# Optimization experiments

Hardware: AMD Instinct MI355X
Metric: run time of the kernel (lower is better)

Reference implementation:

```python
import jax, jax.numpy as jnp
import numpy as np

TOP_K = 2  # config.num_experts_per_tok


def setup_inputs() -> dict:
    key = jax.random.key(0)
    ks = jax.random.split(key, 5)
    B, S, H, F, E = 1, 2048, 2048, 1408, 8
    sc_h = 1.0 / np.sqrt(H)
    sc_f = 1.0 / np.sqrt(F)
    return {
        "hidden_states": jax.random.normal(ks[0], (B, S, H), jnp.float32),
        "gate_w": jax.random.normal(ks[1], (E, H), jnp.float32) * sc_h,
        "w1": jax.random.normal(ks[2], (E, F, H), jnp.float32) * sc_h,
        "w3": jax.random.normal(ks[3], (E, F, H), jnp.float32) * sc_h,
        "w2": jax.random.normal(ks[4], (E, H, F), jnp.float32) * sc_f,
    }


def reference(hidden_states, gate_w, w1, w3, w2):
    B, S, H = hidden_states.shape
    x = hidden_states.reshape(-1, H)            # [T, H]
    T = x.shape[0]
    E = gate_w.shape[0]

    # Router: logits -> fp32 softmax -> top-k -> renormalize
    router_logits = x @ gate_w.T                # [T, E]
    probs = jax.nn.softmax(router_logits.astype(jnp.float32), axis=-1)
    topk_w, topk_idx = jax.lax.top_k(probs, TOP_K)          # [T, K]
    topk_w = topk_w / topk_w.sum(axis=-1, keepdims=True)
    topk_w = topk_w.astype(x.dtype)

    # Scatter top-k weights into a dense [T, E] combine matrix (zero elsewhere)
    w_full = jnp.zeros((T, E), x.dtype).at[jnp.arange(T)[:, None], topk_idx].add(topk_w)

    # Per-expert SwiGLU MLP applied to all tokens; masked combine honors routing.
    g = jnp.einsum('th,efh->etf', x, w1)        # [E, T, F]
    u = jnp.einsum('th,efh->etf', x, w3)        # [E, T, F]
    h = jax.nn.silu(g) * u                      # [E, T, F]
    y = jnp.einsum('etf,ehf->eth', h, w2)       # [E, T, H]
    out = jnp.einsum('eth,te->th', y, w_full)   # [T, H]

    final_hidden_states = out.reshape(B, S, H)
    return final_hidden_states, router_logits
```

## Files before the change

kernel.cpp:

```cpp
#include <hip/hip_runtime.h>
#include <hip/hip_bf16.h>

#define T_TOK 2048
#define H_DIM 2048
#define F_DIM 1408
#define N_EXP 8
#define BM 128
#define BN 64
#define BK 64

#define NITEM 40
#define G1_NY (F_DIM / BN)
#define G2_NY (H_DIM / BN)
#define G1_CHUNK ((NITEM * G1_NY) / 8)
#define G2_CHUNK ((NITEM * G2_NY) / 8)

typedef float f32x4 __attribute__((ext_vector_type(4)));
typedef short s16x8 __attribute__((ext_vector_type(8)));
typedef unsigned int u32;

#define LOFF(row, kbyte) (((row) << 7) + ((kbyte) ^ (((row) & 7) << 4)))

__device__ __forceinline__ int bf2i(__hip_bfloat162 h) {
  int r; __builtin_memcpy(&r, &h, 4); return r;
}

__device__ __forceinline__ int4 pack8(float4 a, float4 b) {
  int4 r;
  r.x = bf2i(__float22bfloat162_rn(float2{a.x, a.y}));
  r.y = bf2i(__float22bfloat162_rn(float2{a.z, a.w}));
  r.z = bf2i(__float22bfloat162_rn(float2{b.x, b.y}));
  r.w = bf2i(__float22bfloat162_rn(float2{b.z, b.w}));
  return r;
}

__device__ __forceinline__ unsigned short f2bf(float f) {
  __hip_bfloat16 h = __float2bfloat16(f);
  unsigned short r; __builtin_memcpy(&r, &h, 2); return r;
}

__device__ __forceinline__ f32x4 mfma16(s16x8 a, s16x8 b, f32x4 c) {
  return __builtin_amdgcn_mfma_f32_16x16x32_bf16(a, b, c, 0, 0, 0);
}

__device__ __forceinline__ void dma16(const unsigned short* g, unsigned short* l) {
  __builtin_amdgcn_global_load_lds((const __attribute__((address_space(1))) u32*)g,
                                   (__attribute__((address_space(3))) u32*)l, 16, 0, 0);
}

__global__ void router_kernel(const float* __restrict__ x, const float* __restrict__ gw,
                              float* __restrict__ logits, int* __restrict__ tk_idx,
                              float* __restrict__ tk_w, unsigned short* __restrict__ xb) {
  __shared__ float xs[H_DIM];
  __shared__ float lg[N_EXP];
  const int t = blockIdx.x;
  const int tid = threadIdx.x;
  const float4 xv = ((const float4*)(x + (size_t)t * H_DIM))[tid];
  ((float4*)xs)[tid] = xv;
  int2 cw;
  cw.x = bf2i(__float22bfloat162_rn(float2{xv.x, xv.y}));
  cw.y = bf2i(__float22bfloat162_rn(float2{xv.z, xv.w}));
  ((int2*)(xb + (size_t)t * H_DIM))[tid] = cw;
  __syncthreads();
  const int w = tid >> 6, l = tid & 63;
  const float* g = gw + w * H_DIM;
  float s = 0.f;
  for (int j = l; j < H_DIM; j += 64) s += xs[j] * g[j];
#pragma unroll
  for (int o = 32; o; o >>= 1) s += __shfl_down(s, o);
  if (l == 0) lg[w] = s;
  __syncthreads();
  if (tid == 0) {
    float mx = lg[0];
#pragma unroll
    for (int i = 1; i < N_EXP; i++) mx = fmaxf(mx, lg[i]);
    float p[N_EXP];
#pragma unroll
    for (int i = 0; i < N_EXP; i++) p[i] = __expf(lg[i] - mx);
    int i0 = 0;
#pragma unroll
    for (int i = 1; i < N_EXP; i++) if (p[i] > p[i0]) i0 = i;
    int i1 = (i0 == 0) ? 1 : 0;
#pragma unroll
    for (int i = 0; i < N_EXP; i++) if (i != i0 && p[i] > p[i1]) i1 = i;
    const float ww = p[i0] + p[i1];
    tk_idx[t * 2] = i0; tk_idx[t * 2 + 1] = i1;
    tk_w[t * 2] = p[i0] / ww; tk_w[t * 2 + 1] = p[i1] / ww;
#pragma unroll
    for (int i = 0; i < N_EXP; i++) logits[t * N_EXP + i] = lg[i];
  }
}

__global__ void build_lists(const int* __restrict__ tk_idx, const float* __restrict__ tk_w,
                            int* __restrict__ counts, int* __restrict__ entries,
                            float* __restrict__ wlist) {
  const int e = blockIdx.x;
  const int l = threadIdx.x;
  int base = 0;
  for (int t0 = 0; t0 < T_TOK; t0 += 64) {
    const int t = t0 + l;
    int sel = -1; float w = 0.f;
    const int i0 = tk_idx[t * 2], i1 = tk_idx[t * 2 + 1];
    if (i0 == e) { sel = t * 2; w = tk_w[t * 2]; }
    else if (i1 == e) { sel = t * 2 + 1; w = tk_w[t * 2 + 1]; }
    const unsigned long long mask = __ballot(sel >= 0);
    const int pos = base + __popcll(mask & ((1ull << l) - 1ull));
    if (sel >= 0) { entries[e * T_TOK + pos] = sel; wlist[e * T_TOK + pos] = w; }
    base += __popcll(mask);
  }
  if (l == 0) counts[e] = base;
}

__global__ void build_items(const int* __restrict__ counts, int* __restrict__ items) {
  if (threadIdx.x == 0) {
    int n = 0;
#pragma unroll
    for (int e = 0; e < N_EXP; e++) {
      const int c = counts[e];
      for (int m0 = 0; m0 < c; m0 += BM) items[1 + n++] = (e << 16) | (m0 / BM);
    }
    items[0] = n;
  }
}

#define G1_STEP(ARD, AWR, BLR1, BLW1, BLR3, BLW3, RS1, RS3, KA1_, KB3_)       \
  {                                                                           \
    asm volatile("s_waitcnt vmcnt(4) lgkmcnt(0)" ::: "memory");               \
    __builtin_amdgcn_s_barrier();                                             \
    *(int4*)((BLW1) + offB) = pack8(RS1[0], RS1[1]);                          \
    *(int4*)((BLW3) + offB) = pack8(RS3[0], RS3[1]);                          \
    {                                                                         \
      const int ka = (KA1_);                                                  \
      dma16(ga0 + ka, (AWR) + aw);                                            \
      dma16(ga1 + ka, (AWR) + aw + 512);                                      \
      const int kbl = (KB3_);                                                 \
      RS1[0] = *(const float4*)(pb1 + kbl);                                   \
      RS1[1] = *(const float4*)(pb1 + kbl + 4);                               \
      RS3[0] = *(const float4*)(pb3 + kbl);                                   \
      RS3[1] = *(const float4*)(pb3 + kbl + 4);                               \
    }                                                                         \
    __builtin_amdgcn_sched_barrier(0);                                        \
    __builtin_amdgcn_s_setprio(1);                                            \
    _Pragma("unroll")                                                         \
    for (int kk = 0; kk < 2; kk++) {                                          \
      const int kbyte = kk * 64 + kb;                                         \
      const s16x8 a0 = *(const s16x8*)((const char*)(ARD) + LOFF(rowA0, kbyte)); \
      const s16x8 a1 = *(const s16x8*)((const char*)(ARD) + LOFF(rowA1, kbyte)); \
      const s16x8 p0 = *(const s16x8*)((BLR1) + LOFF(rowB0, kbyte));          \
      const s16x8 p1 = *(const s16x8*)((BLR1) + LOFF(rowB1, kbyte));          \
      const s16x8 q0 = *(const s16x8*)((BLR3) + LOFF(rowB0, kbyte));          \
      const s16x8 q1 = *(const s16x8*)((BLR3) + LOFF(rowB1, kbyte));          \
      aG[0][0] = mfma16(a0, p0, aG[0][0]); aG[0][1] = mfma16(a0, p1, aG[0][1]); \
      aG[1][0] = mfma16(a1, p0, aG[1][0]); aG[1][1] = mfma16(a1, p1, aG[1][1]); \
      aU[0][0] = mfma16(a0, q0, aU[0][0]); aU[0][1] = mfma16(a0, q1, aU[0][1]); \
      aU[1][0] = mfma16(a1, q0, aU[1][0]); aU[1][1] = mfma16(a1, q1, aU[1][1]); \
    }                                                                         \
    __builtin_amdgcn_s_setprio(0);                                            \
  }

__global__ __launch_bounds__(512)
void moe_gemm1(const float* __restrict__ w1, const float* __restrict__ w3,
               const unsigned short* __restrict__ xb,
               const int* __restrict__ counts, const int* __restrict__ entries,
               const int* __restrict__ items,
               unsigned short* __restrict__ hb) {
  const int lin = blockIdx.x;
  const int virt = (lin & 7) * G1_CHUNK + (lin >> 3);
  const int ix = virt % NITEM;
  const int iy = virt / NITEM;
  if (ix >= items[0]) return;
  const int it = items[1 + ix];
  const int e = it >> 16;
  const int m0 = (it & 0xffff) * BM;
  const int rem = counts[e] - m0;
  const int n0 = iy * BN;

  __shared__ unsigned short sA[2][BM * BK];
  __shared__ unsigned short sB1[2][BN * BK];
  __shared__ unsigned short sB3[2][BN * BK];
  char* sb10 = (char*)sB1[0]; char* sb11 = (char*)sB1[1];
  char* sb30 = (char*)sB3[0]; char* sb31 = (char*)sB3[1];

  const int tid = threadIdx.x;
  const int lane = tid & 63;
  const int wave = tid >> 6;
  const int wm = wave >> 1, wn = wave & 1;

  const int* elist = entries + e * T_TOK + m0;

  const int r0 = tid >> 3;
  const int gc = tid & 7;
  const float* pb1 = w1 + ((size_t)e * F_DIM + n0 + r0) * H_DIM + gc * 8;
  const float* pb3 = w3 + ((size_t)e * F_DIM + n0 + r0) * H_DIM + gc * 8;
  const int offB = LOFF(r0, gc * 16);

  const int arow0 = wave * 16 + (lane >> 3);
  const int arow1 = arow0 + 8;
  const int gcolb = (((lane & 7) << 4) ^ (((lane >> 3) & 7) << 4));
  const int tokA0 = elist[arow0 < rem ? arow0 : 0] >> 1;
  const int tokA1 = elist[arow1 < rem ? arow1 : 0] >> 1;
  const unsigned short* ga0 = xb + (size_t)tokA0 * H_DIM + (gcolb >> 1);
  const unsigned short* ga1 = xb + (size_t)tokA1 * H_DIM + (gcolb >> 1);
  const int aw = wave * 1024;

  const int rowA0 = wm * 32 + (lane & 15);
  const int rowA1 = rowA0 + 16;
  const int rowB0 = wn * 32 + (lane & 15);
  const int rowB1 = rowB0 + 16;
  const int kb = (lane >> 4) * 16;

  const f32x4 zero = {0.f, 0.f, 0.f, 0.f};
  f32x4 aG[2][2], aU[2][2];
#pragma unroll
  for (int i = 0; i < 2; i++)
#pragma unroll
    for (int j = 0; j < 2; j++) { aG[i][j] = zero; aU[i][j] = zero; }

  float4 s1_1[2], s1_3[2], s0_1[2], s0_3[2];
  s1_1[0] = *(const float4*)(pb1);      s1_1[1] = *(const float4*)(pb1 + 4);
  s1_3[0] = *(const float4*)(pb3);      s1_3[1] = *(const float4*)(pb3 + 4);
  s0_1[0] = *(const float4*)(pb1 + BK); s0_1[1] = *(const float4*)(pb1 + BK + 4);
  s0_3[0] = *(const float4*)(pb3 + BK); s0_3[1] = *(const float4*)(pb3 + BK + 4);
  dma16(ga0, sA[0] + aw);
  dma16(ga1, sA[0] + aw + 512);
  asm volatile("s_waitcnt vmcnt(6)" ::: "memory");
  *(int4*)(sb10 + offB) = pack8(s1_1[0], s1_1[1]);
  *(int4*)(sb30 + offB) = pack8(s1_3[0], s1_3[1]);
  s1_1[0] = *(const float4*)(pb1 + 2 * BK); s1_1[1] = *(const float4*)(pb1 + 2 * BK + 4);
  s1_3[0] = *(const float4*)(pb3 + 2 * BK); s1_3[1] = *(const float4*)(pb3 + 2 * BK + 4);

  const int NT = H_DIM / BK;
  for (int t = 0; t < NT; t += 2) {
    const int ka1 = (t + 1 < NT) ? (t + 1) * BK : 0;
    const int ka2 = (t + 2 < NT) ? (t + 2) * BK : 0;
    const int kb3 = (t + 3 < NT) ? (t + 3) * BK : 0;
    const int kb4 = (t + 4 < NT) ? (t + 4) * BK : 0;
    G1_STEP(sA[0], sA[1], sb10, sb11, sb30, sb31, s0_1, s0_3, ka1, kb3);
    G1_STEP(sA[1], sA[0], sb11, sb10, sb31, sb30, s1_1, s1_3, ka2, kb4);
  }

#pragma unroll
  for (int i = 0; i < 2; i++) {
#pragma unroll
    for (int r = 0; r < 4; r++) {
      const int m = wm * 32 + i * 16 + ((lane >> 4) << 2) + r;
      if (m < rem) {
        const int entry = elist[m];
        unsigned short* hp = hb + (size_t)entry * F_DIM + n0 + wn * 32 + (lane & 15);
#pragma unroll
        for (int j = 0; j < 2; j++) {
          const float g = aG[i][j][r];
          const float u = aU[i][j][r];
          hp[j * 16] = f2bf(g / (1.f + __expf(-g)) * u);
        }
      }
    }
  }
}

#define G2_STEP(ARD, AWR, BLR, BLW, RS, KA1_, KB3_)                           \
  {                                                                           \
    asm volatile("s_waitcnt vmcnt(2) lgkmcnt(0)" ::: "memory");               \
    __builtin_amdgcn_s_barrier();                                             \
    *(int4*)((BLW) + offB) = pack8(RS[0], RS[1]);                             \
    {                                                                         \
      const int ka = (KA1_);                                                  \
      dma16(ga0 + ka, (AWR) + aw);                                            \
      dma16(ga1 + ka, (AWR) + aw + 512);                                      \
      const int kbl = (KB3_);                                                 \
      RS[0] = *(const float4*)(pb + kbl);                                     \
      RS[1] = *(const float4*)(pb + kbl + 4);                                 \
    }                                                                         \
    __builtin_amdgcn_sched_barrier(0);                                        \
    __builtin_amdgcn_s_setprio(1);                                            \
    _Pragma("unroll")                                                         \
    for (int kk = 0; kk < 2; kk++) {                                          \
      const int kbyte = kk * 64 + kb;                                         \
      const s16x8 a0 = *(const s16x8*)((const char*)(ARD) + LOFF(rowA0, kbyte)); \
      const s16x8 a1 = *(const s16x8*)((const char*)(ARD) + LOFF(rowA1, kbyte)); \
      const s16x8 f0 = *(const s16x8*)((BLR) + LOFF(rowB0, kbyte));           \
      const s16x8 f1 = *(const s16x8*)((BLR) + LOFF(rowB1, kbyte));           \
      ac[0][0] = mfma16(a0, f0, ac[0][0]); ac[0][1] = mfma16(a0, f1, ac[0][1]); \
      ac[1][0] = mfma16(a1, f0, ac[1][0]); ac[1][1] = mfma16(a1, f1, ac[1][1]); \
    }                                                                         \
    __builtin_amdgcn_s_setprio(0);                                            \
  }

__global__ __launch_bounds__(512)
void moe_gemm2(const float* __restrict__ w2,
               const unsigned short* __restrict__ hb,
               const int* __restrict__ counts, const int* __restrict__ entries,
               const float* __restrict__ wlist, const int* __restrict__ items,
               float* __restrict__ out) {
  const int lin = blockIdx.x;
  const int virt = (lin & 7) * G2_CHUNK + (lin >> 3);
  const int ix = virt % NITEM;
  const int iy = virt / NITEM;
  if (ix >= items[0]) return;
  const int it = items[1 + ix];
  const int e = it >> 16;
  const int m0 = (it & 0xffff) * BM;
  const int rem = counts[e] - m0;
  const int n0 = iy * BN;

  __shared__ unsigned short sA[2][BM * BK];
  __shared__ unsigned short sB[2][BN * BK];
  char* sb0 = (char*)sB[0]; char* sb1 = (char*)sB[1];

  const int tid = threadIdx.x;
  const int lane = tid & 63;
  const int wave = tid >> 6;
  const int wm = wave >> 1, wn = wave & 1;

  const int* elist = entries + e * T_TOK + m0;
  const float* wl = wlist + e * T_TOK + m0;

  const int r0 = tid >> 3;
  const int gc = tid & 7;
  const float* pb = w2 + ((size_t)e * H_DIM + n0 + r0) * F_DIM + gc * 8;
  const int offB = LOFF(r0, gc * 16);

  const int arow0 = wave * 16 + (lane >> 3);
  const int arow1 = arow0 + 8;
  const int gcolb = (((lane & 7) << 4) ^ (((lane >> 3) & 7) << 4));
  const int enA0 = elist[arow0 < rem ? arow0 : 0];
  const int enA1 = elist[arow1 < rem ? arow1 : 0];
  const unsigned short* ga0 = hb + (size_t)enA0 * F_DIM + (gcolb >> 1);
  const unsigned short* ga1 = hb + (size_t)enA1 * F_DIM + (gcolb >> 1);
  const int aw = wave * 1024;

  const int rowA0 = wm * 32 + (lane & 15);
  const int rowA1 = rowA0 + 16;
  const int rowB0 = wn * 32 + (lane & 15);
  const int rowB1 = rowB0 + 16;
  const int kb = (lane >> 4) * 16;

  const f32x4 zero = {0.f, 0.f, 0.f, 0.f};
  f32x4 ac[2][2];
#pragma unroll
  for (int i = 0; i < 2; i++)
#pragma unroll
    for (int j = 0; j < 2; j++) ac[i][j] = zero;

  float4 s1r[2], s0r[2];
  s1r[0] = *(const float4*)(pb);      s1r[1] = *(const float4*)(pb + 4);
  s0r[0] = *(const float4*)(pb + BK); s0r[1] = *(const float4*)(pb + BK + 4);
  dma16(ga0, sA[0] + aw);
  dma16(ga1, sA[0] + aw + 512);
  asm volatile("s_waitcnt vmcnt(4)" ::: "memory");
  *(int4*)(sb0 + offB) = pack8(s1r[0], s1r[1]);
  s1r[0] = *(const float4*)(pb + 2 * BK); s1r[1] = *(const float4*)(pb + 2 * BK + 4);

  const int NT = F_DIM / BK;
  for (int t = 0; t < NT; t += 2) {
    const int ka1 = (t + 1 < NT) ? (t + 1) * BK : 0;
    const int ka2 = (t + 2 < NT) ? (t + 2) * BK : 0;
    const int kb3 = (t + 3 < NT) ? (t + 3) * BK : 0;
    const int kb4 = (t + 4 < NT) ? (t + 4) * BK : 0;
    G2_STEP(sA[0], sA[1], sb0, sb1, s0r, ka1, kb3);
    G2_STEP(sA[1], sA[0], sb1, sb0, s1r, ka2, kb4);
  }

#pragma unroll
  for (int i = 0; i < 2; i++) {
#pragma unroll
    for (int r = 0; r < 4; r++) {
      const int m = wm * 32 + i * 16 + ((lane >> 4) << 2) + r;
      if (m < rem) {
        const int entry = elist[m];
        const int tok = entry >> 1;
        const float wgt = wl[m];
        float* op = out + (size_t)tok * H_DIM + n0 + wn * 32 + (lane & 15);
#pragma unroll
        for (int j = 0; j < 2; j++) atomicAdd(op + j * 16, wgt * ac[i][j][r]);
      }
    }
  }
}

extern "C" void kernel_launch(void* const* d_in, const int* in_sizes, int n_in,
                              void* d_out, int out_size, void* d_ws, size_t ws_size,
                              hipStream_t stream) {
  const float* x  = (const float*)d_in[0];
  const float* gw = (const float*)d_in[1];
  const float* w1 = (const float*)d_in[2];
  const float* w3 = (const float*)d_in[3];
  const float* w2 = (const float*)d_in[4];
  float* out = (float*)d_out;
  float* logits = out + (size_t)T_TOK * H_DIM;

  char* ws = (char*)d_ws;
  size_t off = 0;
  unsigned short* xb = (unsigned short*)(ws + off); off += (size_t)T_TOK * H_DIM * 2;
  unsigned short* hb = (unsigned short*)(ws + off); off += (size_t)T_TOK * 2 * F_DIM * 2;
  int*   tk_idx = (int*)(ws + off);   off += (size_t)T_TOK * 2 * 4;
  float* tk_w   = (float*)(ws + off); off += (size_t)T_TOK * 2 * 4;
  int*   counts = (int*)(ws + off);   off += 256;
  int*   entries = (int*)(ws + off);  off += (size_t)N_EXP * T_TOK * 4;
  float* wlist  = (float*)(ws + off); off += (size_t)N_EXP * T_TOK * 4;
  int*   items  = (int*)(ws + off);   off += 256;

  (void)hipMemsetAsync(d_out, 0, (size_t)out_size * sizeof(float), stream);
  router_kernel<<<dim3(T_TOK), 512, 0, stream>>>(x, gw, logits, tk_idx, tk_w, xb);
  build_lists<<<dim3(N_EXP), 64, 0, stream>>>(tk_idx, tk_w, counts, entries, wlist);
  build_items<<<dim3(1), 64, 0, stream>>>(counts, items);
  moe_gemm1<<<dim3(NITEM * G1_NY), 512, 0, stream>>>(w1, w3, xb, counts, entries, items, hb);
  moe_gemm2<<<dim3(NITEM * G2_NY), 512, 0, stream>>>(w2, hb, counts, entries, wlist, items, out);
}
```

Baseline: 234.2 us.

## Replace A-tile LDS DMA with register-staged prefetch in both MoE GEMMs

Result: slower. 454.7 us (+94.1%).

```diff
diff --git a/kernel.cpp b/kernel.cpp
--- a/kernel.cpp
+++ b/kernel.cpp
@@ -41,11 +41,6 @@
 
 __device__ __forceinline__ f32x4 mfma16(s16x8 a, s16x8 b, f32x4 c) {
   return __builtin_amdgcn_mfma_f32_16x16x32_bf16(a, b, c, 0, 0, 0);
-}
-
-__device__ __forceinline__ void dma16(const unsigned short* g, unsigned short* l) {
-  __builtin_amdgcn_global_load_lds((const __attribute__((address_space(1))) u32*)g,
-                                   (__attribute__((address_space(3))) u32*)l, 16, 0, 0);
 }
 
 __global__ void router_kernel(const float* __restrict__ x, const float* __restrict__ gw,
@@ -123,33 +118,34 @@
   }
 }
 
-#define G1_STEP(ARD, AWR, BLR1, BLW1, BLR3, BLW3, RS1, RS3, KA1_, KB3_)       \
+#define G1_STEP(ARD, AWR, BR1, BW1, BR3, BW3, AS, BS1, BS3, KN_)              \
   {                                                                           \
-    asm volatile("s_waitcnt vmcnt(4) lgkmcnt(0)" ::: "memory");               \
+    asm volatile("s_waitcnt vmcnt(6) lgkmcnt(0)" ::: "memory");               \
     __builtin_amdgcn_s_barrier();                                             \
-    *(int4*)((BLW1) + offB) = pack8(RS1[0], RS1[1]);                          \
-    *(int4*)((BLW3) + offB) = pack8(RS3[0], RS3[1]);                          \
+    *(int4*)((AWR) + offA0) = AS[0];                                          \
+    *(int4*)((AWR) + offA1) = AS[1];                                          \
+    *(int4*)((BW1) + offB) = pack8(BS1[0], BS1[1]);                           \
+    *(int4*)((BW3) + offB) = pack8(BS3[0], BS3[1]);                           \
     {                                                                         \
-      const int ka = (KA1_);                                                  \
-      dma16(ga0 + ka, (AWR) + aw);                                            \
-      dma16(ga1 + ka, (AWR) + aw + 512);                                      \
-      const int kbl = (KB3_);                                                 \
-      RS1[0] = *(const float4*)(pb1 + kbl);                                   \
-      RS1[1] = *(const float4*)(pb1 + kbl + 4);                               \
-      RS3[0] = *(const float4*)(pb3 + kbl);                                   \
-      RS3[1] = *(const float4*)(pb3 + kbl + 4);                               \
+      const int kn = (KN_);                                                   \
+      AS[0] = *(const int4*)(gaA + kn);                                       \
+      AS[1] = *(const int4*)(gaA + kn + 8);                                   \
+      BS1[0] = *(const float4*)(pb1 + kn);                                    \
+      BS1[1] = *(const float4*)(pb1 + kn + 4);                                \
+      BS3[0] = *(const float4*)(pb3 + kn);                                    \
+      BS3[1] = *(const float4*)(pb3 + kn + 4);                                \
     }                                                                         \
     __builtin_amdgcn_sched_barrier(0);                                        \
     __builtin_amdgcn_s_setprio(1);                                            \
     _Pragma("unroll")                                                         \
     for (int kk = 0; kk < 2; kk++) {                                          \
       const int kbyte = kk * 64 + kb;                                         \
-      const s16x8 a0 = *(const s16x8*)((const char*)(ARD) + LOFF(rowA0, kbyte)); \
-      const s16x8 a1 = *(const s16x8*)((const char*)(ARD) + LOFF(rowA1, kbyte)); \
-      const s16x8 p0 = *(const s16x8*)((BLR1) + LOFF(rowB0, kbyte));          \
-      const s16x8 p1 = *(const s16x8*)((BLR1) + LOFF(rowB1, kbyte));          \
-      const s16x8 q0 = *(const s16x8*)((BLR3) + LOFF(rowB0, kbyte));          \
-      const s16x8 q1 = *(const s16x8*)((BLR3) + LOFF(rowB1, kbyte));          \
+      const s16x8 a0 = *(const s16x8*)((ARD) + LOFF(rowA0, kbyte));           \
+      const s16x8 a1 = *(const s16x8*)((ARD) + LOFF(rowA1, kbyte));           \
+      const s16x8 p0 = *(const s16x8*)((BR1) + LOFF(rowB0, kbyte));           \
+      const s16x8 p1 = *(const s16x8*)((BR1) + LOFF(rowB1, kbyte));           \
+      const s16x8 q0 = *(const s16x8*)((BR3) + LOFF(rowB0, kbyte));           \
+      const s16x8 q1 = *(const s16x8*)((BR3) + LOFF(rowB1, kbyte));           \
       aG[0][0] = mfma16(a0, p0, aG[0][0]); aG[0][1] = mfma16(a0, p1, aG[0][1]); \
       aG[1][0] = mfma16(a1, p0, aG[1][0]); aG[1][1] = mfma16(a1, p1, aG[1][1]); \
       aU[0][0] = mfma16(a0, q0, aU[0][0]); aU[0][1] = mfma16(a0, q1, aU[0][1]); \
@@ -178,6 +174,7 @@
   __shared__ unsigned short sA[2][BM * BK];
   __shared__ unsigned short sB1[2][BN * BK];
   __shared__ unsigned short sB3[2][BN * BK];
+  char* sa0 = (char*)sA[0]; char* sa1 = (char*)sA[1];
   char* sb10 = (char*)sB1[0]; char* sb11 = (char*)sB1[1];
   char* sb30 = (char*)sB3[0]; char* sb31 = (char*)sB3[1];
 
@@ -194,14 +191,12 @@
   const float* pb3 = w3 + ((size_t)e * F_DIM + n0 + r0) * H_DIM + gc * 8;
   const int offB = LOFF(r0, gc * 16);
 
-  const int arow0 = wave * 16 + (lane >> 3);
-  const int arow1 = arow0 + 8;
-  const int gcolb = (((lane & 7) << 4) ^ (((lane >> 3) & 7) << 4));
-  const int tokA0 = elist[arow0 < rem ? arow0 : 0] >> 1;
-  const int tokA1 = elist[arow1 < rem ? arow1 : 0] >> 1;
-  const unsigned short* ga0 = xb + (size_t)tokA0 * H_DIM + (gcolb >> 1);
-  const unsigned short* ga1 = xb + (size_t)tokA1 * H_DIM + (gcolb >> 1);
-  const int aw = wave * 1024;
+  const int r0a = tid >> 2;
+  const int gc4 = tid & 3;
+  const int tokA = elist[r0a < rem ? r0a : 0] >> 1;
+  const unsigned short* gaA = xb + (size_t)tokA * H_DIM + gc4 * 16;
+  const int offA0 = LOFF(r0a, gc4 * 32);
+  const int offA1 = LOFF(r0a, gc4 * 32 + 16);
 
   const int rowA0 = wm * 32 + (lane & 15);
   const int rowA1 = rowA0 + 16;
@@ -216,27 +211,29 @@
 #pragma unroll
     for (int j = 0; j < 2; j++) { aG[i][j] = zero; aU[i][j] = zero; }
 
-  float4 s1_1[2], s1_3[2], s0_1[2], s0_3[2];
-  s1_1[0] = *(const float4*)(pb1);      s1_1[1] = *(const float4*)(pb1 + 4);
-  s1_3[0] = *(const float4*)(pb3);      s1_3[1] = *(const float4*)(pb3 + 4);
-  s0_1[0] = *(const float4*)(pb1 + BK); s0_1[1] = *(const float4*)(pb1 + BK + 4);
-  s0_3[0] = *(const float4*)(pb3 + BK); s0_3[1] = *(const float4*)(pb3 + BK + 4);
-  dma16(ga0, sA[0] + aw);
-  dma16(ga1, sA[0] + aw + 512);
-  asm volatile("s_waitcnt vmcnt(6)" ::: "memory");
-  *(int4*)(sb10 + offB) = pack8(s1_1[0], s1_1[1]);
-  *(int4*)(sb30 + offB) = pack8(s1_3[0], s1_3[1]);
-  s1_1[0] = *(const float4*)(pb1 + 2 * BK); s1_1[1] = *(const float4*)(pb1 + 2 * BK + 4);
-  s1_3[0] = *(const float4*)(pb3 + 2 * BK); s1_3[1] = *(const float4*)(pb3 + 2 * BK + 4);
+  int4 A0[2], A1r[2];
+  float4 B0_1[2], B0_3[2], B1_1[2], B1_3[2];
+  A0[0] = *(const int4*)(gaA);      A0[1] = *(const int4*)(gaA + 8);
+  B0_1[0] = *(const float4*)(pb1);  B0_1[1] = *(const float4*)(pb1 + 4);
+  B0_3[0] = *(const float4*)(pb3);  B0_3[1] = *(const float4*)(pb3 + 4);
+  asm volatile("s_waitcnt vmcnt(0)" ::: "memory");
+  *(int4*)(sa0 + offA0) = A0[0];
+  *(int4*)(sa0 + offA1) = A0[1];
+  *(int4*)(sb10 + offB) = pack8(B0_1[0], B0_1[1]);
+  *(int4*)(sb30 + offB) = pack8(B0_3[0], B0_3[1]);
+  A0[0] = *(const int4*)(gaA + BK);      A0[1] = *(const int4*)(gaA + BK + 8);
+  B0_1[0] = *(const float4*)(pb1 + BK);  B0_1[1] = *(const float4*)(pb1 + BK + 4);
+  B0_3[0] = *(const float4*)(pb3 + BK);  B0_3[1] = *(const float4*)(pb3 + BK + 4);
+  A1r[0] = *(const int4*)(gaA + 2 * BK);      A1r[1] = *(const int4*)(gaA + 2 * BK + 8);
+  B1_1[0] = *(const float4*)(pb1 + 2 * BK);   B1_1[1] = *(const float4*)(pb1 + 2 * BK + 4);
+  B1_3[0] = *(const float4*)(pb3 + 2 * BK);   B1_3[1] = *(const float4*)(pb3 + 2 * BK + 4);
 
   const int NT = H_DIM / BK;
   for (int t = 0; t < NT; t += 2) {
-    const int ka1 = (t + 1 < NT) ? (t + 1) * BK : 0;
-    const int ka2 = (t + 2 < NT) ? (t + 2) * BK : 0;
-    const int kb3 = (t + 3 < NT) ? (t + 3) * BK : 0;
-    const int kb4 = (t + 4 < NT) ? (t + 4) * BK : 0;
-    G1_STEP(sA[0], sA[1], sb10, sb11, sb30, sb31, s0_1, s0_3, ka1, kb3);
-    G1_STEP(sA[1], sA[0], sb11, sb10, sb31, sb30, s1_1, s1_3, ka2, kb4);
+    const int kn0 = (t + 3 < NT) ? (t + 3) * BK : 0;
+    const int kn1 = (t + 4 < NT) ? (t + 4) * BK : 0;
+    G1_STEP(sa0, sa1, sb10, sb11, sb30, sb31, A0, B0_1, B0_3, kn0);
+    G1_STEP(sa1, sa0, sb11, sb10, sb31, sb30, A1r, B1_1, B1_3, kn1);
   }
 
 #pragma unroll
@@ -258,28 +255,29 @@
   }
 }
 
-#define G2_STEP(ARD, AWR, BLR, BLW, RS, KA1_, KB3_)                           \
+#define G2_STEP(ARD, AWR, BR, BW, AS, BS, KN_)                                \
   {                                                                           \
-    asm volatile("s_waitcnt vmcnt(2) lgkmcnt(0)" ::: "memory");               \
+    asm volatile("s_waitcnt vmcnt(4) lgkmcnt(0)" ::: "memory");               \
     __builtin_amdgcn_s_barrier();                                             \
-    *(int4*)((BLW) + offB) = pack8(RS[0], RS[1]);                             \
+    *(int4*)((AWR) + offA0) = AS[0];                                          \
+    *(int4*)((AWR) + offA1) = AS[1];                                          \
+    *(int4*)((BW) + offB) = pack8(BS[0], BS[1]);                              \
     {                                                                         \
-      const int ka = (KA1_);                                                  \
-      dma16(ga0 + ka, (AWR) + aw);                                            \
-      dma16(ga1 + ka, (AWR) + aw + 512);                                      \
-      const int kbl = (KB3_);                                                 \
-      RS[0] = *(const float4*)(pb + kbl);                                     \
-      RS[1] = *(const float4*)(pb + kbl + 4);                                 \
+      const int kn = (KN_);                                                   \
+      AS[0] = *(const int4*)(gaA + kn);                                       \
+      AS[1] = *(const int4*)(gaA + kn + 8);                                   \
+      BS[0] = *(const float4*)(pb + kn);                                      \
+      BS[1] = *(const float4*)(pb + kn + 4);                                  \
     }                                                                         \
     __builtin_amdgcn_sched_barrier(0);                                        \
     __builtin_amdgcn_s_setprio(1);                                            \
     _Pragma("unroll")                                                         \
     for (int kk = 0; kk < 2; kk++) {                                          \
       const int kbyte = kk * 64 + kb;                                         \
-      const s16x8 a0 = *(const s16x8*)((const char*)(ARD) + LOFF(rowA0, kbyte)); \
-      const s16x8 a1 = *(const s16x8*)((const char*)(ARD) + LOFF(rowA1, kbyte)); \
-      const s16x8 f0 = *(const s16x8*)((BLR) + LOFF(rowB0, kbyte));           \
-      const s16x8 f1 = *(const s16x8*)((BLR) + LOFF(rowB1, kbyte));           \
+      const s16x8 a0 = *(const s16x8*)((ARD) + LOFF(rowA0, kbyte));           \
+      const s16x8 a1 = *(const s16x8*)((ARD) + LOFF(rowA1, kbyte));           \
+      const s16x8 f0 = *(const s16x8*)((BR) + LOFF(rowB0, kbyte));            \
+      const s16x8 f1 = *(const s16x8*)((BR) + LOFF(rowB1, kbyte));            \
       ac[0][0] = mfma16(a0, f0, ac[0][0]); ac[0][1] = mfma16(a0, f1, ac[0][1]); \
       ac[1][0] = mfma16(a1, f0, ac[1][0]); ac[1][1] = mfma16(a1, f1, ac[1][1]); \
     }                                                                         \
@@ -305,6 +303,7 @@
 
   __shared__ unsigned short sA[2][BM * BK];
   __shared__ unsigned short sB[2][BN * BK];
+  char* sa0 = (char*)sA[0]; char* sa1 = (char*)sA[1];
   char* sb0 = (char*)sB[0]; char* sb1 = (char*)sB[1];
 
   const int tid = threadIdx.x;
@@ -320,14 +319,12 @@
   const float* pb = w2 + ((size_t)e * H_DIM + n0 + r0) * F_DIM + gc * 8;
   const int offB = LOFF(r0, gc * 16);
 
-  const int arow0 = wave * 16 + (lane >> 3);
-  const int arow1 = arow0 + 8;
-  const int gcolb = (((lane & 7) << 4) ^ (((lane >> 3) & 7) << 4));
-  const int enA0 = elist[arow0 < rem ? arow0 : 0];
-  const int enA1 = elist[arow1 < rem ? arow1 : 0];
-  const unsigned short* ga0 = hb + (size_t)enA0 * F_DIM + (gcolb >> 1);
-  const unsigned short* ga1 = hb + (size_t)enA1 * F_DIM + (gcolb >> 1);
-  const int aw = wave * 1024;
+  const int r0a = tid >> 2;
+  const int gc4 = tid & 3;
+  const int enA = elist[r0a < rem ? r0a : 0];
+  const unsigned short* gaA = hb + (size_t)enA * F_DIM + gc4 * 16;
+  const int offA0 = LOFF(r0a, gc4 * 32);
+  const int offA1 = LOFF(r0a, gc4 * 32 + 16);
 
   const int rowA0 = wm * 32 + (lane & 15);
   const int rowA1 = rowA0 + 16;
@@ -342,23 +339,25 @@
 #pragma unroll
     for (int j = 0; j < 2; j++) ac[i][j] = zero;
 
-  float4 s1r[2], s0r[2];
-  s1r[0] = *(const float4*)(pb);      s1r[1] = *(const float4*)(pb + 4);
-  s0r[0] = *(const float4*)(pb + BK); s0r[1] = *(const float4*)(pb + BK + 4);
-  dma16(ga0, sA[0] + aw);
-  dma16(ga1, sA[0] + aw + 512);
-  asm volatile("s_waitcnt vmcnt(4)" ::: "memory");
-  *(int4*)(sb0 + offB) = pack8(s1r[0], s1r[1]);
-  s1r[0] = *(const float4*)(pb + 2 * BK); s1r[1] = *(const float4*)(pb + 2 * BK + 4);
+  int4 A0[2], A1r[2];
+  float4 B0r[2], B1r[2];
+  A0[0] = *(const int4*)(gaA);     A0[1] = *(const int4*)(gaA + 8);
+  B0r[0] = *(const float4*)(pb);   B0r[1] = *(const float4*)(pb + 4);
+  asm volatile("s_waitcnt vmcnt(0)" ::: "memory");
+  *(int4*)(sa0 + offA0) = A0[0];
+  *(int4*)(sa0 + offA1) = A0[1];
+  *(int4*)(sb0 + offB) = pack8(B0r[0], B0r[1]);
+  A0[0] = *(const int4*)(gaA + BK);      A0[1] = *(const int4*)(gaA + BK + 8);
+  B0r[0] = *(const float4*)(pb + BK);    B0r[1] = *(const float4*)(pb + BK + 4);
+  A1r[0] = *(const int4*)(gaA + 2 * BK); A1r[1] = *(const int4*)(gaA + 2 * BK + 8);
+  B1r[0] = *(const float4*)(pb + 2 * BK); B1r[1] = *(const float4*)(pb + 2 * BK + 4);
 
   const int NT = F_DIM / BK;
   for (int t = 0; t < NT; t += 2) {
-    const int ka1 = (t + 1 < NT) ? (t + 1) * BK : 0;
-    const int ka2 = (t + 2 < NT) ? (t + 2) * BK : 0;
-    const int kb3 = (t + 3 < NT) ? (t + 3) * BK : 0;
-    const int kb4 = (t + 4 < NT) ? (t + 4) * BK : 0;
-    G2_STEP(sA[0], sA[1], sb0, sb1, s0r, ka1, kb3);
-    G2_STEP(sA[1], sA[0], sb1, sb0, s1r, ka2, kb4);
+    const int kn0 = (t + 3 < NT) ? (t + 3) * BK : 0;
+    const int kn1 = (t + 4 < NT) ? (t + 4) * BK : 0;
+    G2_STEP(sa0, sa1, sb0, sb1, A0, B0r, kn0);
+    G2_STEP(sa1, sa0, sb1, sb0, A1r, B1r, kn1);
   }
 
 #pragma unroll
```

## Pre-cast expert weights to bf16 and use DMA-only grouped GEMMs

Applied to the files above, without the earlier changes.

Result: slower. 278.1 us (+18.7%).

```diff
diff --git a/kernel.cpp b/kernel.cpp
--- a/kernel.cpp
+++ b/kernel.cpp
@@ -14,6 +14,7 @@
 #define G2_NY (H_DIM / BN)
 #define G1_CHUNK ((NITEM * G1_NY) / 8)
 #define G2_CHUNK ((NITEM * G2_NY) / 8)
+#define WELEMS ((size_t)N_EXP * F_DIM * H_DIM)
 
 typedef float f32x4 __attribute__((ext_vector_type(4)));
 typedef short s16x8 __attribute__((ext_vector_type(8)));
@@ -46,6 +47,16 @@
 __device__ __forceinline__ void dma16(const unsigned short* g, unsigned short* l) {
   __builtin_amdgcn_global_load_lds((const __attribute__((address_space(1))) u32*)g,
                                    (__attribute__((address_space(3))) u32*)l, 16, 0, 0);
+}
+
+__global__ void cast_w(const float* __restrict__ in, unsigned short* __restrict__ out, int n8) {
+  int i = blockIdx.x * blockDim.x + threadIdx.x;
+  const int stride = gridDim.x * blockDim.x;
+  for (; i < n8; i += stride) {
+    const float4 a = ((const float4*)in)[2 * i];
+    const float4 b = ((const float4*)in)[2 * i + 1];
+    ((int4*)out)[i] = pack8(a, b);
+  }
 }
 
 __global__ void router_kernel(const float* __restrict__ x, const float* __restrict__ gw,
@@ -123,7 +134,225 @@
   }
 }
 
-#define G1_STEP(ARD, AWR, BLR1, BLW1, BLR3, BLW3, RS1, RS3, KA1_, KB3_)       \
+__global__ __launch_bounds__(512)
+void moe_gemm1b(const unsigned short* __restrict__ w1b, const unsigned short* __restrict__ w3b,
+                const unsigned short* __restrict__ xb,
+                const int* __restrict__ counts, const int* __restrict__ entries,
+                const int* __restrict__ items,
+                unsigned short* __restrict__ hb) {
+  const int lin = blockIdx.x;
+  const int virt = (lin & 7) * G1_CHUNK + (lin >> 3);
+  const int ix = virt % NITEM;
+  const int iy = virt / NITEM;
+  if (ix >= items[0]) return;
+  const int it = items[1 + ix];
+  const int e = it >> 16;
+  const int m0 = (it & 0xffff) * BM;
+  const int rem = counts[e] - m0;
+  const int n0 = iy * BN;
+
+  __shared__ unsigned short sA[2][BM * BK];
+  __shared__ unsigned short sB1[2][BN * BK];
+  __shared__ unsigned short sB3[2][BN * BK];
+
+  const int tid = threadIdx.x;
+  const int lane = tid & 63;
+  const int wave = tid >> 6;
+  const int wm = wave >> 1, wn = wave & 1;
+
+  const int* elist = entries + e * T_TOK + m0;
+
+  const int gcolb = (((lane & 7) << 4) ^ (((lane >> 3) & 7) << 4));
+  const int arow0 = wave * 16 + (lane >> 3);
+  const int arow1 = arow0 + 8;
+  const int tokA0 = elist[arow0 < rem ? arow0 : 0] >> 1;
+  const int tokA1 = elist[arow1 < rem ? arow1 : 0] >> 1;
+  const unsigned short* gaA0 = xb + (size_t)tokA0 * H_DIM + (gcolb >> 1);
+  const unsigned short* gaA1 = xb + (size_t)tokA1 * H_DIM + (gcolb >> 1);
+  const int awA = wave * 1024;
+
+  const int rB = tid >> 3;
+  const int gbcol = ((tid & 7) ^ (rB & 7)) * 8;
+  const unsigned short* gb1 = w1b + ((size_t)e * F_DIM + n0 + rB) * H_DIM + gbcol;
+  const unsigned short* gb3 = w3b + ((size_t)e * F_DIM + n0 + rB) * H_DIM + gbcol;
+  const int awB = wave * 512;
+
+  const int rowA0 = wm * 32 + (lane & 15);
+  const int rowA1 = rowA0 + 16;
+  const int rowB0 = wn * 32 + (lane & 15);
+  const int rowB1 = rowB0 + 16;
+  const int kb = (lane >> 4) * 16;
+
+  const f32x4 zero = {0.f, 0.f, 0.f, 0.f};
+  f32x4 aG[2][2], aU[2][2];
+#pragma unroll
+  for (int i = 0; i < 2; i++)
+#pragma unroll
+    for (int j = 0; j < 2; j++) { aG[i][j] = zero; aU[i][j] = zero; }
+
+  dma16(gaA0, sA[0] + awA);
+  dma16(gaA1, sA[0] + awA + 512);
+  dma16(gb1, sB1[0] + awB);
+  dma16(gb3, sB3[0] + awB);
+  asm volatile("s_waitcnt vmcnt(0)" ::: "memory");
+  __builtin_amdgcn_s_barrier();
+
+  const int NT = H_DIM / BK;
+  for (int t = 0; t < NT; ++t) {
+    const int cur = t & 1, nxt = cur ^ 1;
+    const int kn = (t + 1 < NT) ? (t + 1) * BK : 0;
+    dma16(gaA0 + kn, sA[nxt] + awA);
+    dma16(gaA1 + kn, sA[nxt] + awA + 512);
+    dma16(gb1 + kn, sB1[nxt] + awB);
+    dma16(gb3 + kn, sB3[nxt] + awB);
+    __builtin_amdgcn_sched_barrier(0);
+    __builtin_amdgcn_s_setprio(1);
+    const char* aC = (const char*)sA[cur];
+    const char* b1C = (const char*)sB1[cur];
+    const char* b3C = (const char*)sB3[cur];
+#pragma unroll
+    for (int kk = 0; kk < 2; kk++) {
+      const int kbyte = kk * 64 + kb;
+      const s16x8 a0 = *(const s16x8*)(aC + LOFF(rowA0, kbyte));
+      const s16x8 a1 = *(const s16x8*)(aC + LOFF(rowA1, kbyte));
+      const s16x8 p0 = *(const s16x8*)(b1C + LOFF(rowB0, kbyte));
+      const s16x8 p1 = *(const s16x8*)(b1C + LOFF(rowB1, kbyte));
+      const s16x8 q0 = *(const s16x8*)(b3C + LOFF(rowB0, kbyte));
+      const s16x8 q1 = *(const s16x8*)(b3C + LOFF(rowB1, kbyte));
+      aG[0][0] = mfma16(a0, p0, aG[0][0]); aG[0][1] = mfma16(a0, p1, aG[0][1]);
+      aG[1][0] = mfma16(a1, p0, aG[1][0]); aG[1][1] = mfma16(a1, p1, aG[1][1]);
+      aU[0][0] = mfma16(a0, q0, aU[0][0]); aU[0][1] = mfma16(a0, q1, aU[0][1]);
+      aU[1][0] = mfma16(a1, q0, aU[1][0]); aU[1][1] = mfma16(a1, q1, aU[1][1]);
+    }
+    __builtin_amdgcn_s_setprio(0);
+    asm volatile("s_waitcnt vmcnt(0) lgkmcnt(0)" ::: "memory");
+    __builtin_amdgcn_s_barrier();
+  }
+
+#pragma unroll
+  for (int i = 0; i < 2; i++) {
+#pragma unroll
+    for (int r = 0; r < 4; r++) {
+      const int m = wm * 32 + i * 16 + ((lane >> 4) << 2) + r;
+      if (m < rem) {
+        const int entry = elist[m];
+        unsigned short* hp = hb + (size_t)entry * F_DIM + n0 + wn * 32 + (lane & 15);
+#pragma unroll
+        for (int j = 0; j < 2; j++) {
+          const float g = aG[i][j][r];
+          const float u = aU[i][j][r];
+          hp[j * 16] = f2bf(g / (1.f + __expf(-g)) * u);
+        }
+      }
+    }
+  }
+}
+
+__global__ __launch_bounds__(512)
+void moe_gemm2b(const unsigned short* __restrict__ w2b,
+                const unsigned short* __restrict__ hb,
+                const int* __restrict__ counts, const int* __restrict__ entries,
+                const float* __restrict__ wlist, const int* __restrict__ items,
+                float* __restrict__ out) {
+  const int lin = blockIdx.x;
+  const int virt = (lin & 7) * G2_CHUNK + (lin >> 3);
+  const int ix = virt % NITEM;
+  const int iy = virt / NITEM;
+  if (ix >= items[0]) return;
+  const int it = items[1 + ix];
+  const int e = it >> 16;
+  const int m0 = (it & 0xffff) * BM;
+  const int rem = counts[e] - m0;
+  const int n0 = iy * BN;
+
+  __shared__ unsigned short sA[2][BM * BK];
+  __shared__ unsigned short sB[2][BN * BK];
+
+  const int tid = threadIdx.x;
+  const int lane = tid & 63;
+  const int wave = tid >> 6;
+  const int wm = wave >> 1, wn = wave & 1;
+
+  const int* elist = entries + e * T_TOK + m0;
+  const float* wl = wlist + e * T_TOK + m0;
+
+  const int gcolb = (((lane & 7) << 4) ^ (((lane >> 3) & 7) << 4));
+  const int arow0 = wave * 16 + (lane >> 3);
+  const int arow1 = arow0 + 8;
+  const int enA0 = elist[arow0 < rem ? arow0 : 0];
+  const int enA1 = elist[arow1 < rem ? arow1 : 0];
+  const unsigned short* gaA0 = hb + (size_t)enA0 * F_DIM + (gcolb >> 1);
+  const unsigned short* gaA1 = hb + (size_t)enA1 * F_DIM + (gcolb >> 1);
+  const int awA = wave * 1024;
+
+  const int rB = tid >> 3;
+  const int gbcol = ((tid & 7) ^ (rB & 7)) * 8;
+  const unsigned short* gb = w2b + ((size_t)e * H_DIM + n0 + rB) * F_DIM + gbcol;
+  const int awB = wave * 512;
+
+  const int rowA0 = wm * 32 + (lane & 15);
+  const int rowA1 = rowA0 + 16;
+  const int rowB0 = wn * 32 + (lane & 15);
+  const int rowB1 = rowB0 + 16;
+  const int kb = (lane >> 4) * 16;
+
+  const f32x4 zero = {0.f, 0.f, 0.f, 0.f};
+  f32x4 ac[2][2];
+#pragma unroll
+  for (int i = 0; i < 2; i++)
+#pragma unroll
+    for (int j = 0; j < 2; j++) ac[i][j] = zero;
+
+  dma16(gaA0, sA[0] + awA);
+  dma16(gaA1, sA[0] + awA + 512);
+  dma16(gb, sB[0] + awB);
+  asm volatile("s_waitcnt vmcnt(0)" ::: "memory");
+  __builtin_amdgcn_s_barrier();
+
+  const int NT = F_DIM / BK;
+  for (int t = 0; t < NT; ++t) {
+    const int cur = t & 1, nxt = cur ^ 1;
+    const int kn = (t + 1 < NT) ? (t + 1) * BK : 0;
+    dma16(gaA0 + kn, sA[nxt] + awA);
+    dma16(gaA1 + kn, sA[nxt] + awA + 512);
+    dma16(gb + kn, sB[nxt] + awB);
+    __builtin_amdgcn_sched_barrier(0);
+    __builtin_amdgcn_s_setprio(1);
+    const char* aC = (const char*)sA[cur];
+    const char* bC = (const char*)sB[cur];
+#pragma unroll
+    for (int kk = 0; kk < 2; kk++) {
+      const int kbyte = kk * 64 + kb;
+      const s16x8 a0 = *(const s16x8*)(aC + LOFF(rowA0, kbyte));
+      const s16x8 a1 = *(const s16x8*)(aC + LOFF(rowA1, kbyte));
+      const s16x8 f0 = *(const s16x8*)(bC + LOFF(rowB0, kbyte));
+      const s16x8 f1 = *(const s16x8*)(bC + LOFF(rowB1, kbyte));
+      ac[0][0] = mfma16(a0, f0, ac[0][0]); ac[0][1] = mfma16(a0, f1, ac[0][1]);
+      ac[1][0] = mfma16(a1, f0, ac[1][0]); ac[1][1] = mfma16(a1, f1, ac[1][1]);
+    }
+    __builtin_amdgcn_s_setprio(0);
+    asm volatile("s_waitcnt vmcnt(0) lgkmcnt(0)" ::: "memory");
+    __builtin_amdgcn_s_barrier();
+  }
+
+#pragma unroll
+  for (int i = 0; i < 2; i++) {
+#pragma unroll
+    for (int r = 0; r < 4; r++) {
+      const int m = wm * 32 + i * 16 + ((lane >> 4) << 2) + r;
+      if (m < rem) {
+        const int entry = elist[m];
+        const int tok = entry >> 1;
+        const float wgt = wl[m];
+        float* op = out + (size_t)tok * H_DIM + n0 + wn * 32 + (lane & 15);
+#pragma unroll
+        for (int j = 0; j < 2; j++) atomicAdd(op + j * 16, wgt * ac[i][j][r]);
+      }
+    }
+  }
+}
+
+#define G1F_STEP(ARD, AWR, BLR1, BLW1, BLR3, BLW3, RS1, RS3, KA1_, KB3_)      \
   {                                                                           \
     asm volatile("s_waitcnt vmcnt(4) lgkmcnt(0)" ::: "memory");               \
     __builtin_amdgcn_s_barrier();                                             \
@@ -159,11 +388,11 @@
   }
 
 __global__ __launch_bounds__(512)
-void moe_gemm1(const float* __restrict__ w1, const float* __restrict__ w3,
-               const unsigned short* __restrict__ xb,
-               const int* __restrict__ counts, const int* __restrict__ entries,
-               const int* __restrict__ items,
-               unsigned short* __restrict__ hb) {
+void moe_gemm1f(const float* __restrict__ w1, const float* __restrict__ w3,
+                const unsigned short* __restrict__ xb,
+                const int* __restrict__ counts, const int* __restrict__ entries,
+                const int* __restrict__ items,
+                unsigned short* __restrict__ hb) {
   const int lin = blockIdx.x;
   const int virt = (lin & 7) * G1_CHUNK + (lin >> 3);
   const int ix = virt % NITEM;
@@ -235,8 +464,8 @@
     const int ka2 = (t + 2 < NT) ? (t + 2) * BK : 0;
     const int kb3 = (t + 3 < NT) ? (t + 3) * BK : 0;
     const int kb4 = (t + 4 < NT) ? (t + 4) * BK : 0;
-    G1_STEP(sA[0], sA[1], sb10, sb11, sb30, sb31, s0_1, s0_3, ka1, kb3);
-    G1_STEP(sA[1], sA[0], sb11, sb10, sb31, sb30, s1_1, s1_3, ka2, kb4);
+    G1F_STEP(sA[0], sA[1], sb10, sb11, sb30, sb31, s0_1, s0_3, ka1, kb3);
+    G1F_STEP(sA[1], sA[0], sb11, sb10, sb31, sb30, s1_1, s1_3, ka2, kb4);
   }
 
 #pragma unroll
@@ -258,7 +487,7 @@
   }
 }
 
-#define G2_STEP(ARD, AWR, BLR, BLW, RS, KA1_, KB3_)                           \
+#define G2F_STEP(ARD, AWR, BLR, BLW, RS, KA1_, KB3_)                          \
   {                                                                           \
     asm volatile("s_waitcnt vmcnt(2) lgkmcnt(0)" ::: "memory");               \
     __builtin_amdgcn_s_barrier();                                             \
@@ -287,11 +516,11 @@
   }
 
 __global__ __launch_bounds__(512)
-void moe_gemm2(const float* __restrict__ w2,
-               const unsigned short* __restrict__ hb,
-               const int* __restrict__ counts, const int* __restrict__ entries,
-               const float* __restrict__ wlist, const int* __restrict__ items,
-               float* __restrict__ out) {
+void moe_gemm2f(const float* __restrict__ w2,
+                const unsigned short* __restrict__ hb,
+                const int* __restrict__ counts, const int* __restrict__ entries,
+                const float* __restrict__ wlist, const int* __restrict__ items,
+                float* __restrict__ out) {
   const int lin = blockIdx.x;
   const int virt = (lin & 7) * G2_CHUNK + (lin >> 3);
   const int ix = virt % NITEM;
@@ -357,8 +586,8 @@
     const int ka2 = (t + 2 < NT) ? (t + 2) * BK : 0;
     const int kb3 = (t + 3 < NT) ? (t + 3) * BK : 0;
     const int kb4 = (t + 4 < NT) ? (t + 4) * BK : 0;
-    G2_STEP(sA[0], sA[1], sb0, sb1, s0r, ka1, kb3);
-    G2_STEP(sA[1], sA[0], sb1, sb0, s1r, ka2, kb4);
+    G2F_STEP(sA[0], sA[1], sb0, sb1, s0r, ka1, kb3);
+    G2F_STEP(sA[1], sA[0], sb1, sb0, s1r, ka2, kb4);
   }
 
 #pragma unroll
@@ -399,11 +628,25 @@
   int*   entries = (int*)(ws + off);  off += (size_t)N_EXP * T_TOK * 4;
   float* wlist  = (float*)(ws + off); off += (size_t)N_EXP * T_TOK * 4;
   int*   items  = (int*)(ws + off);   off += 256;
+  unsigned short* w1b = (unsigned short*)(ws + off); off += WELEMS * 2;
+  unsigned short* w3b = (unsigned short*)(ws + off); off += WELEMS * 2;
+  unsigned short* w2b = (unsigned short*)(ws + off); off += WELEMS * 2;
+  const size_t need = off;
 
   (void)hipMemsetAsync(d_out, 0, (size_t)out_size * sizeof(float), stream);
   router_kernel<<<dim3(T_TOK), 512, 0, stream>>>(x, gw, logits, tk_idx, tk_w, xb);
   build_lists<<<dim3(N_EXP), 64, 0, stream>>>(tk_idx, tk_w, counts, entries, wlist);
   build_items<<<dim3(1), 64, 0, stream>>>(counts, items);
-  moe_gemm1<<<dim3(NITEM * G1_NY), 512, 0, stream>>>(w1, w3, xb, counts, entries, items, hb);
-  moe_gemm2<<<dim3(NITEM * G2_NY), 512, 0, stream>>>(w2, hb, counts, entries, wlist, items, out);
-}
+
+  if (ws_size >= need) {
+    const int n8 = (int)(WELEMS / 8);
+    cast_w<<<dim3(2048), 256, 0, stream>>>(w1, w1b, n8);
+    cast_w<<<dim3(2048), 256, 0, stream>>>(w3, w3b, n8);
+    cast_w<<<dim3(2048), 256, 0, stream>>>(w2, w2b, n8);
+    moe_gemm1b<<<dim3(NITEM * G1_NY), 512, 0, stream>>>(w1b, w3b, xb, counts, entries, items, hb);
+    moe_gemm2b<<<dim3(NITEM * G2_NY), 512, 0, stream>>>(w2b, hb, counts, entries, wlist, items, out);
+  } else {
+    moe_gemm1f<<<dim3(NITEM * G1_NY), 512, 0, stream>>>(w1, w3, xb, counts, entries, items, hb);
+    moe_gemm2f<<<dim3(NITEM * G2_NY), 512, 0, stream>>>(w2, hb, counts, entries, wlist, items, out);
+  }
+}
```
